# Performance work log

Measured on AMD Instinct MI355X. Metric: run time of the kernel, lower is better.

## Reference

```python
import jax, jax.numpy as jnp
import numpy as np

N_NODES = 50000
N_EDGES = 800000
IN_C = 128
OUT_C = 128
NEG_SLOPE = 0.2  # leaky_relu alpha


def setup_inputs() -> dict:
    key = jax.random.key(0)
    k1, k2, k3, k4 = jax.random.split(key, 4)
    h = jax.random.normal(k1, (N_NODES, IN_C), dtype=jnp.float32)
    edge_index = jax.random.randint(k2, (2, N_EDGES), 0, N_NODES, dtype=jnp.int64)
    # xavier_uniform with gain=1.414
    gW = 1.414 * np.sqrt(6.0 / (IN_C + OUT_C))
    W = jax.random.uniform(k3, (IN_C, OUT_C), dtype=jnp.float32, minval=-gW, maxval=gW)
    ga = 1.414 * np.sqrt(6.0 / (2 * OUT_C + 1))
    a = jax.random.uniform(k4, (2 * OUT_C, 1), dtype=jnp.float32, minval=-ga, maxval=ga)
    return {"h": h, "edge_index": edge_index, "W": W, "a": a}


def reference(h, edge_index, W, a):
    # eval mode (no dropout), concat=True -> ELU output
    Wh = h @ W                                  # [N, F]
    row, col = edge_index[0], edge_index[1]     # source, target
    F_out = W.shape[1]
    # cat([Wh_i, Wh_j]) @ a  ==  (Wh @ a_src)[row] + (Wh @ a_dst)[col]
    alpha_src = Wh @ a[:F_out, 0]               # [N]
    alpha_dst = Wh @ a[F_out:, 0]               # [N]
    edge_e = jax.nn.leaky_relu(alpha_src[row] + alpha_dst[col], negative_slope=NEG_SLOPE)  # [E]
    n = Wh.shape[0]
    # segment softmax over incoming edges of each target node
    m = jax.ops.segment_max(edge_e, col, num_segments=n)       # [N] (-inf for empty, never indexed)
    exp_e = jnp.exp(edge_e - m[col])                            # [E]
    s = jax.ops.segment_sum(exp_e, col, num_segments=n)         # [N]
    attn = exp_e / (s[col] + 1e-16)                              # [E]
    # scatter-add aggregation of attended source features
    h_prime = jax.ops.segment_sum(Wh[row] * attn[:, None], col, num_segments=n)  # [N, F]
    return jax.nn.elu(h_prime)
```

## Files before the change

kernel.cpp:

```cpp
#include <hip/hip_runtime.h>
#include <math.h>

#define NEG_BIG -1.0e30f
#define BSHIFT 8
#define MAXB 256

typedef __attribute__((ext_vector_type(8))) short short8v;
typedef __attribute__((ext_vector_type(4))) float f32x4;

__device__ __forceinline__ ushort f2bf(float f) {
  unsigned u = __float_as_uint(f);
  unsigned r = (u + 0x7fffu + ((u >> 16) & 1u)) >> 16;
  return (ushort)r;
}
__device__ __forceinline__ float bf_lo(unsigned u) { return __uint_as_float(u << 16); }
__device__ __forceinline__ float bf_hi(unsigned u) { return __uint_as_float(u & 0xffff0000u); }

__global__ void wprep_k(const float* __restrict__ W, ushort* __restrict__ Wbf,
                        int* __restrict__ bucket_count, int* __restrict__ done) {
  int j = blockIdx.x * blockDim.x + threadIdx.x;
  if (j < MAXB) bucket_count[j] = 0;
  if (j == 0) *done = 0;
  if (j >= 128 * 128) return;
  int i = j & 7;
  int l = (j >> 3) & 63;
  int n0 = (j >> 9) & 7;
  int kk = j >> 12;
  int k = kk * 32 + ((l >> 4) & 3) * 8 + i;
  int n = n0 * 16 + (l & 15);
  Wbf[j] = f2bf(W[k * 128 + n]);
}

__global__ __launch_bounds__(256) void histB_k(const void* __restrict__ ei, int E,
                                               unsigned* __restrict__ packed,
                                               int* __restrict__ bucket_count,
                                               int* __restrict__ done,
                                               int* __restrict__ bcur,
                                               int* __restrict__ bucket_base, int nblocks) {
  __shared__ int lh[MAXB];
  __shared__ int wsum[4];
  __shared__ int last;
  int tid = (int)threadIdx.x;
  lh[tid] = 0;
  __syncthreads();

  const int* p32 = (const int*)ei;
  bool is64 = true;
#pragma unroll
  for (int i = 0; i < 32; ++i) is64 = is64 && (p32[2 * i + 1] == 0);
  const long long* p64 = (const long long*)ei;
  int stride = gridDim.x * 256;
  for (int e = blockIdx.x * 256 + tid; e < E; e += stride) {
    int r, c;
    if (is64) { r = (int)p64[e]; c = (int)p64[E + e]; }
    else      { r = p32[e];      c = p32[E + e]; }
    packed[e] = ((unsigned)c << 16) | (unsigned)r;
    atomicAdd(&lh[c >> BSHIFT], 1);
  }
  __syncthreads();
  if (lh[tid]) atomicAdd(&bucket_count[tid], lh[tid]);
  __threadfence();
  if (tid == 0) {
    int old = atomicAdd(done, 1);
    last = (old == nblocks - 1);
  }
  __syncthreads();
  if (!last) return;
  __threadfence();

  int lane = tid & 63, wid = tid >> 6;
  int v = atomicAdd(&bucket_count[tid], 0);
  int x = v;
#pragma unroll
  for (int off = 1; off < 64; off <<= 1) {
    int t = __shfl_up(x, off);
    if (lane >= off) x += t;
  }
  if (lane == 63) wsum[wid] = x;
  __syncthreads();
  int woff = 0;
  for (int w = 0; w < wid; ++w) woff += wsum[w];
  int excl = woff + x - v;
  bcur[tid] = excl;
  bucket_base[tid] = excl;
  if (tid == 255) bucket_base[256] = excl + v;
}

__global__ __launch_bounds__(256) void gemm_wh(const float* __restrict__ h,
                                               const ushort* __restrict__ Wbf,
                                               const float* __restrict__ a,
                                               ushort* __restrict__ Whb,
                                               float* __restrict__ asrc,
                                               float* __restrict__ adst, int N) {
  int tid = (int)threadIdx.x;
  int w = tid >> 6;
  int l = tid & 63;
  int lg = l >> 4;
  int lm = l & 15;
  int r0 = blockIdx.x * 64 + 16 * w;
  const short8v* Wb8 = (const short8v*)Wbf;

  float as_v[8], ad_v[8];
#pragma unroll
  for (int n0 = 0; n0 < 8; ++n0) {
    as_v[n0] = a[n0 * 16 + lm];
    ad_v[n0] = a[128 + n0 * 16 + lm];
  }

  f32x4 acc[8];
#pragma unroll
  for (int n0 = 0; n0 < 8; ++n0) acc[n0] = (f32x4){0.f, 0.f, 0.f, 0.f};

  int arow = r0 + lm;
  const float* hrow = h + (size_t)arow * 128;
  bool rok = (arow < N);

#pragma unroll
  for (int kk = 0; kk < 4; ++kk) {
    short8v av;
    if (rok) {
      const float4* hp = (const float4*)(hrow + kk * 32 + lg * 8);
      float4 x0 = hp[0], x1 = hp[1];
      av[0] = (short)f2bf(x0.x); av[1] = (short)f2bf(x0.y);
      av[2] = (short)f2bf(x0.z); av[3] = (short)f2bf(x0.w);
      av[4] = (short)f2bf(x1.x); av[5] = (short)f2bf(x1.y);
      av[6] = (short)f2bf(x1.z); av[7] = (short)f2bf(x1.w);
    } else {
      av = (short8v){0, 0, 0, 0, 0, 0, 0, 0};
    }
#pragma unroll
    for (int n0 = 0; n0 < 8; ++n0) {
      short8v bv = Wb8[(kk * 8 + n0) * 64 + l];
      acc[n0] = __builtin_amdgcn_mfma_f32_16x16x32_bf16(av, bv, acc[n0], 0, 0, 0);
    }
  }

#pragma unroll
  for (int reg = 0; reg < 4; ++reg) {
    int r = r0 + lg * 4 + reg;
    if (r < N) {
      ushort* dst = Whb + (size_t)r * 128;
#pragma unroll
      for (int n0 = 0; n0 < 8; ++n0) dst[n0 * 16 + lm] = f2bf(acc[n0][reg]);
    }
  }

#pragma unroll
  for (int reg = 0; reg < 4; ++reg) {
    float ps = 0.f, pd = 0.f;
#pragma unroll
    for (int n0 = 0; n0 < 8; ++n0) {
      ps += acc[n0][reg] * as_v[n0];
      pd += acc[n0][reg] * ad_v[n0];
    }
#pragma unroll
    for (int off = 1; off < 16; off <<= 1) {
      ps += __shfl_xor(ps, off);
      pd += __shfl_xor(pd, off);
    }
    int r = r0 + lg * 4 + reg;
    if (lm == 0 && r < N) { asrc[r] = ps; adst[r] = pd; }
  }
}

#define TILE 8192
__global__ __launch_bounds__(1024) void bin_k(const unsigned* __restrict__ packed,
                                              int* __restrict__ bcur,
                                              unsigned* __restrict__ bin_buf, int E) {
  __shared__ int lhist[MAXB];
  __shared__ int lbase[MAXB];
  int tid = (int)threadIdx.x;
  int t0 = blockIdx.x * TILE;

  if (tid < MAXB) lhist[tid] = 0;
  __syncthreads();

  unsigned rec[8];
  int rb[8], rr[8];
#pragma unroll
  for (int k = 0; k < 8; ++k) {
    int i = t0 + tid + k * 1024;
    rb[k] = -1;
    if (i < E) {
      rec[k] = packed[i];
      rb[k] = (int)(rec[k] >> (16 + BSHIFT));
      rr[k] = atomicAdd(&lhist[rb[k]], 1);
    }
  }
  __syncthreads();
  if (tid < MAXB) lbase[tid] = lhist[tid] ? atomicAdd(&bcur[tid], lhist[tid]) : 0;
  __syncthreads();
#pragma unroll
  for (int k = 0; k < 8; ++k) {
    if (rb[k] >= 0) bin_buf[lbase[rb[k]] + rr[k]] = rec[k];
  }
}

__global__ __launch_bounds__(1024) void perm3_k(const unsigned* __restrict__ bin_buf,
                                                const int* __restrict__ bucket_base,
                                                int* __restrict__ rowptr,
                                                ushort* __restrict__ row_sorted,
                                                int N, int nbuckets) {
  __shared__ int hist[MAXB];
  __shared__ int cur[MAXB];
  __shared__ int wsum[16];
  int b = blockIdx.x;
  int tid = (int)threadIdx.x;
  int c0 = b << BSHIFT;
  int ncol = min(MAXB, N - c0);
  int e0 = bucket_base[b], e1 = bucket_base[b + 1];

  if (tid < MAXB) hist[tid] = 0;
  __syncthreads();
  for (int i = e0 + tid; i < e1; i += 1024)
    atomicAdd(&hist[(bin_buf[i] >> 16) - c0], 1);
  __syncthreads();

  int lane = tid & 63, wid = tid >> 6;
  int v = (tid < MAXB) ? hist[tid] : 0;
  int x = v;
#pragma unroll
  for (int off = 1; off < 64; off <<= 1) {
    int t = __shfl_up(x, off);
    if (lane >= off) x += t;
  }
  if (lane == 63) wsum[wid] = x;
  __syncthreads();
  if (tid < MAXB) {
    int woff = 0;
    for (int w = 0; w < wid; ++w) woff += wsum[w];
    int excl = woff + x - v;
    cur[tid] = e0 + excl;
    if (tid < ncol) rowptr[c0 + tid] = e0 + excl;
  }
  if (b == nbuckets - 1 && tid == 0) rowptr[N] = e1;
  __syncthreads();

  for (int i = e0 + tid; i < e1; i += 1024) {
    unsigned rec = bin_buf[i];
    int p = atomicAdd(&cur[(rec >> 16) - c0], 1);
    row_sorted[p] = (ushort)(rec & 0xffffu);
  }
}

__global__ __launch_bounds__(256) void softagg_k(const int* __restrict__ rowptr,
                                                 const ushort* __restrict__ row_sorted,
                                                 const float* __restrict__ asrc,
                                                 const float* __restrict__ adst,
                                                 const ushort* __restrict__ Whb,
                                                 float* __restrict__ out, int N) {
  int node = blockIdx.x * 4 + ((int)threadIdx.x >> 6);
  if (node >= N) return;
  int lane = (int)threadIdx.x & 63;
  int beg = rowptr[node], end = rowptr[node + 1];
  int deg = end - beg;
  float adc = adst[node];
  float ax = 0.f, ay = 0.f;

  if (deg <= 64) {
    int r = 0;
    float v = NEG_BIG;
    if (lane < deg) {
      r = row_sorted[beg + lane];
      v = asrc[r] + adc;
      v = (v >= 0.f) ? v : 0.2f * v;
    }
    float m = v;
#pragma unroll
    for (int off = 32; off > 0; off >>= 1) m = fmaxf(m, __shfl_xor(m, off));
    float e = (lane < deg) ? expf(v - m) : 0.f;
    float s = e;
#pragma unroll
    for (int off = 32; off > 0; off >>= 1) s += __shfl_xor(s, off);
    float w = e / (s + 1e-16f);

    int j = 0;
    for (; j + 3 < deg; j += 4) {
      float w0 = __shfl(w, j), w1 = __shfl(w, j + 1), w2 = __shfl(w, j + 2), w3 = __shfl(w, j + 3);
      int r0 = __shfl(r, j), r1 = __shfl(r, j + 1), r2 = __shfl(r, j + 2), r3 = __shfl(r, j + 3);
      unsigned u0 = ((const unsigned*)(Whb + (size_t)r0 * 128))[lane];
      unsigned u1 = ((const unsigned*)(Whb + (size_t)r1 * 128))[lane];
      unsigned u2 = ((const unsigned*)(Whb + (size_t)r2 * 128))[lane];
      unsigned u3 = ((const unsigned*)(Whb + (size_t)r3 * 128))[lane];
      ax += w0 * bf_lo(u0); ay += w0 * bf_hi(u0);
      ax += w1 * bf_lo(u1); ay += w1 * bf_hi(u1);
      ax += w2 * bf_lo(u2); ay += w2 * bf_hi(u2);
      ax += w3 * bf_lo(u3); ay += w3 * bf_hi(u3);
    }
    for (; j < deg; ++j) {
      float wj = __shfl(w, j);
      int rj = __shfl(r, j);
      unsigned u = ((const unsigned*)(Whb + (size_t)rj * 128))[lane];
      ax += wj * bf_lo(u); ay += wj * bf_hi(u);
    }
  } else {
    float m = NEG_BIG, s = 0.f;
    for (int i = beg + lane; i < end; i += 64) {
      float v = asrc[row_sorted[i]] + adc;
      v = (v >= 0.f) ? v : 0.2f * v;
      if (v > m) { s = s * expf(m - v) + 1.f; m = v; }
      else       { s += expf(v - m); }
    }
#pragma unroll
    for (int off = 32; off > 0; off >>= 1) {
      float mo = __shfl_xor(m, off);
      float so = __shfl_xor(s, off);
      float M = fmaxf(m, mo);
      s = s * expf(m - M) + so * expf(mo - M);
      m = M;
    }
    float inv = 1.f / (s + 1e-16f);
    for (int i = beg; i < end; ++i) {
      int rj = row_sorted[i];
      float v = asrc[rj] + adc;
      v = (v >= 0.f) ? v : 0.2f * v;
      float wj = expf(v - m) * inv;
      unsigned u = ((const unsigned*)(Whb + (size_t)rj * 128))[lane];
      ax += wj * bf_lo(u); ay += wj * bf_hi(u);
    }
  }

  ax = ax > 0.f ? ax : expm1f(ax);
  ay = ay > 0.f ? ay : expm1f(ay);
  ((float2*)out)[(size_t)node * 64 + lane] = make_float2(ax, ay);
}

extern "C" void kernel_launch(void* const* d_in, const int* in_sizes, int n_in,
                              void* d_out, int out_size, void* d_ws, size_t ws_size,
                              hipStream_t stream) {
  const float* h = (const float*)d_in[0];
  const void* ei = d_in[1];
  const float* W = (const float*)d_in[2];
  const float* a = (const float*)d_in[3];
  int N = in_sizes[0] / 128;
  int E = in_sizes[1] / 2;
  float* out = (float*)d_out;

  ushort* Whb = (ushort*)d_ws;
  float* asrc = (float*)(Whb + (size_t)N * 128);
  float* adst = asrc + N;
  int* bucket_count = (int*)(adst + N);
  int* done = bucket_count + MAXB;
  int* bcur = done + 4;
  int* bucket_base = bcur + MAXB;
  int* rowptr = bucket_base + MAXB + 4;
  unsigned* bin_buf = (unsigned*)(rowptr + N + 1);
  unsigned* packed = bin_buf + E;
  ushort* row_sorted = (ushort*)(packed + E);
  ushort* Wbf = row_sorted + E;

  int nbuckets = (N + MAXB - 1) >> BSHIFT;
  const int HBLOCKS = 256;

  wprep_k<<<64, 256, 0, stream>>>(W, Wbf, bucket_count, done);
  histB_k<<<HBLOCKS, 256, 0, stream>>>(ei, E, packed, bucket_count, done, bcur, bucket_base, HBLOCKS);
  gemm_wh<<<(N + 63) / 64, 256, 0, stream>>>(h, Wbf, a, Whb, asrc, adst, N);
  bin_k<<<(E + TILE - 1) / TILE, 1024, 0, stream>>>(packed, bcur, bin_buf, E);
  perm3_k<<<nbuckets, 1024, 0, stream>>>(bin_buf, bucket_base, rowptr, row_sorted, N, nbuckets);
  softagg_k<<<(N + 3) / 4, 256, 0, stream>>>(rowptr, row_sorted, asrc, adst, Whb, out, N);
}
```

Measured before the change: 105.0 us.

## Stage W and h tiles in LDS inside GEMM, halve bin tile, unroll gather by eight

The separate W-to-bf16 prep kernel is replaced by a tiny zeroing kernel. Each GEMM block now converts the full W matrix and its 64-row h tile into MFMA-fragment layout in shared memory, which gives coalesced global loads. The binning kernel processes 4096 edges per block instead of 8192, so it launches more blocks. The aggregation gather loop is unrolled from 4 to 8 neighbor rows to keep more loads in flight. In exchange, every GEMM block redundantly converts W (64 KB of fp32 reads per block), which adds work and LDS pressure.

```diff
diff --git a/kernel.cpp b/kernel.cpp
--- a/kernel.cpp
+++ b/kernel.cpp
@@ -16,19 +16,10 @@
 __device__ __forceinline__ float bf_lo(unsigned u) { return __uint_as_float(u << 16); }
 __device__ __forceinline__ float bf_hi(unsigned u) { return __uint_as_float(u & 0xffff0000u); }
 
-__global__ void wprep_k(const float* __restrict__ W, ushort* __restrict__ Wbf,
-                        int* __restrict__ bucket_count, int* __restrict__ done) {
-  int j = blockIdx.x * blockDim.x + threadIdx.x;
-  if (j < MAXB) bucket_count[j] = 0;
-  if (j == 0) *done = 0;
-  if (j >= 128 * 128) return;
-  int i = j & 7;
-  int l = (j >> 3) & 63;
-  int n0 = (j >> 9) & 7;
-  int kk = j >> 12;
-  int k = kk * 32 + ((l >> 4) & 3) * 8 + i;
-  int n = n0 * 16 + (l & 15);
-  Wbf[j] = f2bf(W[k * 128 + n]);
+__global__ void zero_k(int* __restrict__ bucket_count, int* __restrict__ done) {
+  int t = (int)threadIdx.x;
+  if (t < MAXB) bucket_count[t] = 0;
+  if (t == 0) *done = 0;
 }
 
 __global__ __launch_bounds__(256) void histB_k(const void* __restrict__ ei, int E,
@@ -87,18 +78,52 @@
 }
 
 __global__ __launch_bounds__(256) void gemm_wh(const float* __restrict__ h,
-                                               const ushort* __restrict__ Wbf,
+                                               const float* __restrict__ W,
                                                const float* __restrict__ a,
                                                ushort* __restrict__ Whb,
                                                float* __restrict__ asrc,
                                                float* __restrict__ adst, int N) {
+  __shared__ ushort Af[4 * 4 * 64 * 8];
+  __shared__ ushort Bf[4 * 8 * 64 * 8];
   int tid = (int)threadIdx.x;
+  int r0 = blockIdx.x * 64;
+
+  for (int idx = tid; idx < 4096; idx += 256) {
+    float4 v = ((const float4*)W)[idx];
+    int k = idx >> 5;
+    int n4 = (idx & 31) * 4;
+    int kk = k >> 5, lg = (k & 31) >> 3, i = k & 7;
+    int n0 = n4 >> 4, lm0 = n4 & 15;
+    int slot = ((kk * 8 + n0) * 64 + lg * 16 + lm0) * 8 + i;
+    Bf[slot]      = f2bf(v.x);
+    Bf[slot + 8]  = f2bf(v.y);
+    Bf[slot + 16] = f2bf(v.z);
+    Bf[slot + 24] = f2bf(v.w);
+  }
+
+  for (int idx = tid; idx < 2048; idx += 256) {
+    int row = idx >> 5;
+    int c4 = idx & 31;
+    int gr = r0 + row;
+    float4 v = (gr < N) ? ((const float4*)h)[(size_t)gr * 32 + c4]
+                        : make_float4(0.f, 0.f, 0.f, 0.f);
+    int c0 = c4 * 4;
+    int w = row >> 4, lm = row & 15;
+    int kk = c0 >> 5, lg = (c0 & 31) >> 3, i0 = c0 & 7;
+    int slotbase = ((w * 4 + kk) * 64 + lg * 16 + lm) * 8 + i0;
+    ushort4 pk;
+    pk.x = f2bf(v.x); pk.y = f2bf(v.y); pk.z = f2bf(v.z); pk.w = f2bf(v.w);
+    *(ushort4*)&Af[slotbase] = pk;
+  }
+  __syncthreads();
+
   int w = tid >> 6;
   int l = tid & 63;
   int lg = l >> 4;
   int lm = l & 15;
-  int r0 = blockIdx.x * 64 + 16 * w;
-  const short8v* Wb8 = (const short8v*)Wbf;
+  int r0w = r0 + 16 * w;
+  const short8v* Af8 = (const short8v*)Af;
+  const short8v* Bf8 = (const short8v*)Bf;
 
   float as_v[8], ad_v[8];
 #pragma unroll
@@ -111,33 +136,19 @@
 #pragma unroll
   for (int n0 = 0; n0 < 8; ++n0) acc[n0] = (f32x4){0.f, 0.f, 0.f, 0.f};
 
-  int arow = r0 + lm;
-  const float* hrow = h + (size_t)arow * 128;
-  bool rok = (arow < N);
-
 #pragma unroll
   for (int kk = 0; kk < 4; ++kk) {
-    short8v av;
-    if (rok) {
-      const float4* hp = (const float4*)(hrow + kk * 32 + lg * 8);
-      float4 x0 = hp[0], x1 = hp[1];
-      av[0] = (short)f2bf(x0.x); av[1] = (short)f2bf(x0.y);
-      av[2] = (short)f2bf(x0.z); av[3] = (short)f2bf(x0.w);
-      av[4] = (short)f2bf(x1.x); av[5] = (short)f2bf(x1.y);
-      av[6] = (short)f2bf(x1.z); av[7] = (short)f2bf(x1.w);
-    } else {
-      av = (short8v){0, 0, 0, 0, 0, 0, 0, 0};
-    }
+    short8v av = Af8[(w * 4 + kk) * 64 + l];
 #pragma unroll
     for (int n0 = 0; n0 < 8; ++n0) {
-      short8v bv = Wb8[(kk * 8 + n0) * 64 + l];
+      short8v bv = Bf8[(kk * 8 + n0) * 64 + l];
       acc[n0] = __builtin_amdgcn_mfma_f32_16x16x32_bf16(av, bv, acc[n0], 0, 0, 0);
     }
   }
 
 #pragma unroll
   for (int reg = 0; reg < 4; ++reg) {
-    int r = r0 + lg * 4 + reg;
+    int r = r0w + lg * 4 + reg;
     if (r < N) {
       ushort* dst = Whb + (size_t)r * 128;
 #pragma unroll
@@ -158,12 +169,12 @@
       ps += __shfl_xor(ps, off);
       pd += __shfl_xor(pd, off);
     }
-    int r = r0 + lg * 4 + reg;
+    int r = r0w + lg * 4 + reg;
     if (lm == 0 && r < N) { asrc[r] = ps; adst[r] = pd; }
   }
 }
 
-#define TILE 8192
+#define TILE 4096
 __global__ __launch_bounds__(1024) void bin_k(const unsigned* __restrict__ packed,
                                               int* __restrict__ bcur,
                                               unsigned* __restrict__ bin_buf, int E) {
@@ -175,10 +186,10 @@
   if (tid < MAXB) lhist[tid] = 0;
   __syncthreads();
 
-  unsigned rec[8];
-  int rb[8], rr[8];
-#pragma unroll
-  for (int k = 0; k < 8; ++k) {
+  unsigned rec[4];
+  int rb[4], rr[4];
+#pragma unroll
+  for (int k = 0; k < 4; ++k) {
     int i = t0 + tid + k * 1024;
     rb[k] = -1;
     if (i < E) {
@@ -191,7 +202,7 @@
   if (tid < MAXB) lbase[tid] = lhist[tid] ? atomicAdd(&bcur[tid], lhist[tid]) : 0;
   __syncthreads();
 #pragma unroll
-  for (int k = 0; k < 8; ++k) {
+  for (int k = 0; k < 4; ++k) {
     if (rb[k] >= 0) bin_buf[lbase[rb[k]] + rr[k]] = rec[k];
   }
 }
@@ -275,17 +286,16 @@
     float w = e / (s + 1e-16f);
 
     int j = 0;
-    for (; j + 3 < deg; j += 4) {
-      float w0 = __shfl(w, j), w1 = __shfl(w, j + 1), w2 = __shfl(w, j + 2), w3 = __shfl(w, j + 3);
-      int r0 = __shfl(r, j), r1 = __shfl(r, j + 1), r2 = __shfl(r, j + 2), r3 = __shfl(r, j + 3);
-      unsigned u0 = ((const unsigned*)(Whb + (size_t)r0 * 128))[lane];
-      unsigned u1 = ((const unsigned*)(Whb + (size_t)r1 * 128))[lane];
-      unsigned u2 = ((const unsigned*)(Whb + (size_t)r2 * 128))[lane];
-      unsigned u3 = ((const unsigned*)(Whb + (size_t)r3 * 128))[lane];
-      ax += w0 * bf_lo(u0); ay += w0 * bf_hi(u0);
-      ax += w1 * bf_lo(u1); ay += w1 * bf_hi(u1);
-      ax += w2 * bf_lo(u2); ay += w2 * bf_hi(u2);
-      ax += w3 * bf_lo(u3); ay += w3 * bf_hi(u3);
+    for (; j + 7 < deg; j += 8) {
+      float wv[8];
+      int rv[8];
+#pragma unroll
+      for (int q = 0; q < 8; ++q) { wv[q] = __shfl(w, j + q); rv[q] = __shfl(r, j + q); }
+      unsigned u[8];
+#pragma unroll
+      for (int q = 0; q < 8; ++q) u[q] = ((const unsigned*)(Whb + (size_t)rv[q] * 128))[lane];
+#pragma unroll
+      for (int q = 0; q < 8; ++q) { ax += wv[q] * bf_lo(u[q]); ay += wv[q] * bf_hi(u[q]); }
     }
     for (; j < deg; ++j) {
       float wj = __shfl(w, j);
@@ -347,14 +357,13 @@
   unsigned* bin_buf = (unsigned*)(rowptr + N + 1);
   unsigned* packed = bin_buf + E;
   ushort* row_sorted = (ushort*)(packed + E);
-  ushort* Wbf = row_sorted + E;
 
   int nbuckets = (N + MAXB - 1) >> BSHIFT;
   const int HBLOCKS = 256;
 
-  wprep_k<<<64, 256, 0, stream>>>(W, Wbf, bucket_count, done);
+  zero_k<<<1, 256, 0, stream>>>(bucket_count, done);
   histB_k<<<HBLOCKS, 256, 0, stream>>>(ei, E, packed, bucket_count, done, bcur, bucket_base, HBLOCKS);
-  gemm_wh<<<(N + 63) / 64, 256, 0, stream>>>(h, Wbf, a, Whb, asrc, adst, N);
+  gemm_wh<<<(N + 63) / 64, 256, 0, stream>>>(h, W, a, Whb, asrc, adst, N);
   bin_k<<<(E + TILE - 1) / TILE, 1024, 0, stream>>>(packed, bcur, bin_buf, E);
   perm3_k<<<nbuckets, 1024, 0, stream>>>(bin_buf, bucket_base, rowptr, row_sorted, N, nbuckets);
   softagg_k<<<(N + 3) / 4, 256, 0, stream>>>(rowptr, row_sorted, asrc, adst, Whb, out, N);
```

After: 117.1 us. 1.12x slower.
